# Kernel tuning notes

Hardware: AMD Instinct MI355X
Metric: run time of the kernel (lower is better)

The kernel has to match this reference:

```python
import jax, jax.numpy as jnp
import numpy as np

FEAT = 512
MATCH = 256
EPS = 1e-5

def layernorm(x, gamma, beta):
    mu = jnp.mean(x, axis=-1, keepdims=True)
    var = jnp.var(x, axis=-1, keepdims=True)
    return (x - mu) * jax.lax.rsqrt(var + EPS) * gamma + beta

def setup_inputs() -> dict:
    key = jax.random.key(0)
    ks = jax.random.split(key, 5)
    B, N = 8, 2048
    patch_corr_map = jax.random.normal(ks[0], (B, N, FEAT), dtype=jnp.float32)
    W_proj = jax.random.normal(ks[1], (FEAT, MATCH), dtype=jnp.float32) * (1.0 / np.sqrt(FEAT))
    b_proj = jnp.zeros((MATCH,), dtype=jnp.float32)
    g1 = jnp.ones((MATCH,), dtype=jnp.float32)
    be1 = jnp.zeros((MATCH,), dtype=jnp.float32)
    g2 = jnp.ones((FEAT,), dtype=jnp.float32)
    be2 = jnp.zeros((FEAT,), dtype=jnp.float32)
    W_out = jax.random.normal(ks[2], (FEAT, FEAT), dtype=jnp.float32) * (1.0 / np.sqrt(FEAT))
    b_out = jnp.zeros((FEAT,), dtype=jnp.float32)
    return {"patch_corr_map": patch_corr_map, "W_proj": W_proj, "b_proj": b_proj,
            "g1": g1, "be1": be1, "g2": g2, "be2": be2, "W_out": W_out, "b_out": b_out}

def reference(patch_corr_map, W_proj, b_proj, g1, be1, g2, be2, W_out, b_out):
    # Linear feat->match, then LayerNorm; q = k = normed projection
    proj = jnp.einsum('bnf,fm->bnm', patch_corr_map, W_proj) + b_proj
    qk = layernorm(proj, g1, be1)                      # [B,N,M]
    v = layernorm(patch_corr_map, g2, be2)             # [B,N,F]
    attn = jnp.einsum('bnm,bkm->bnk', qk, qk)          # [B,N,N], no scaling (matches torch)
    attn = jax.nn.softmax(attn, axis=-1)
    out = jnp.einsum('bnk,bkf->bnf', attn, v)          # [B,N,F]
    out = out + (jnp.einsum('bnf,fg->bng', out, W_out) + b_out)
    return out
```

## Files before the change

kernel.cpp:

```cpp
#include <hip/hip_runtime.h>
#include <hip/hip_bf16.h>
#include <cstdint>
#include <cstddef>

#define FEAT 512
#define MATCH 256
#define NB 8
#define NSEQ 2048
#define NROWS (NB*NSEQ)
#define LN_EPS 1e-5f

using f32x4  = __attribute__((ext_vector_type(4))) float;
using bf16x8 = __attribute__((ext_vector_type(8))) short;
using s16x4  = __attribute__((ext_vector_type(4))) short;
using i32x4  = __attribute__((ext_vector_type(4))) int;

__device__ __forceinline__ float bf2f(short h){
  return __builtin_bit_cast(float, (uint32_t)((uint32_t)(uint16_t)h << 16));
}
__device__ __forceinline__ short f2bf(float f){
  uint32_t u = __builtin_bit_cast(uint32_t, f);
  u += 0x7FFFu + ((u >> 16) & 1u);
  return (short)(u >> 16);
}
__device__ __forceinline__ int cvtpk(float a, float b){
  int d;
  asm("v_cvt_pk_bf16_f32 %0, %1, %2" : "=v"(d) : "v"(a), "v"(b));
  return d;
}
__device__ __forceinline__ void gl_lds16(const void* g, void* l){
  __builtin_amdgcn_global_load_lds(
    (const __attribute__((address_space(1))) uint32_t*)g,
    (__attribute__((address_space(3))) uint32_t*)l, 16, 0, 0);
}
#define MFMA16(a,b,c) __builtin_amdgcn_mfma_f32_16x16x32_bf16((a),(b),(c),0,0,0)

template<int ADDI>
__global__ void k_transpose_convert(const float* __restrict__ src, short* __restrict__ dst,
                                    int R, int C){
  __shared__ short tile[32][33];
  int tx = threadIdx.x, ty = threadIdx.y;
  int c0 = blockIdx.x * 32, r0 = blockIdx.y * 32;
#pragma unroll
  for (int r = 0; r < 4; r++){
    int gr = r0 + ty + 8*r, gc = c0 + tx;
    float v = src[(size_t)gr * C + gc];
    if (ADDI && gr == gc) v += 1.0f;
    tile[ty + 8*r][tx] = f2bf(v);
  }
  __syncthreads();
#pragma unroll
  for (int r = 0; r < 4; r++)
    dst[(size_t)(c0 + ty + 8*r) * R + r0 + tx] = tile[tx][ty + 8*r];
}

__launch_bounds__(512)
__global__ void k_prep2(const float* __restrict__ x, const float* __restrict__ g2,
                        const float* __restrict__ be2,
                        short* __restrict__ xbf, short* __restrict__ vT){
  __shared__ short vtile[32*FEAT];
  int t = threadIdx.x, l = t & 63, w = t >> 6;
  int b  = blockIdx.x >> 6;
  int n0 = (blockIdx.x & 63) * 32;
  float4 ga = ((const float4*)g2)[l*2],  gb = ((const float4*)g2)[l*2+1];
  float4 ea = ((const float4*)be2)[l*2], eb = ((const float4*)be2)[l*2+1];
#pragma unroll
  for (int r = 0; r < 4; r++){
    int rowL = w*4 + r;
    size_t row = (size_t)b * NSEQ + n0 + rowL;
    const float* xr = x + row * FEAT;
    float4 a = ((const float4*)xr)[l*2];
    float4 c = ((const float4*)xr)[l*2+1];
    float s  = a.x+a.y+a.z+a.w + c.x+c.y+c.z+c.w;
    float ss = a.x*a.x+a.y*a.y+a.z*a.z+a.w*a.w + c.x*c.x+c.y*c.y+c.z*c.z+c.w*c.w;
#pragma unroll
    for (int d = 1; d < 64; d <<= 1){ s += __shfl_xor(s, d); ss += __shfl_xor(ss, d); }
    float mu  = s * (1.f/FEAT);
    float var = ss * (1.f/FEAT) - mu*mu;
    float rs  = rsqrtf(var + LN_EPS);
    bf16x8 xv, vv;
    float xs[8] = {a.x,a.y,a.z,a.w,c.x,c.y,c.z,c.w};
    float gs[8] = {ga.x,ga.y,ga.z,ga.w,gb.x,gb.y,gb.z,gb.w};
    float es[8] = {ea.x,ea.y,ea.z,ea.w,eb.x,eb.y,eb.z,eb.w};
#pragma unroll
    for (int i = 0; i < 8; i++){
      xv[i] = f2bf(xs[i]);
      vv[i] = f2bf((xs[i]-mu)*rs*gs[i] + es[i]);
    }
    *(bf16x8*)(xbf + row*FEAT + l*8) = xv;
    *(bf16x8*)(vtile + rowL*FEAT + l*8) = vv;
  }
  __syncthreads();
  short col[32];
#pragma unroll
  for (int n = 0; n < 32; n++) col[n] = vtile[n*FEAT + t];
  short* dst = vT + (size_t)b * FEAT * NSEQ + (size_t)t * NSEQ + n0;
#pragma unroll
  for (int c = 0; c < 4; c++)
    *(bf16x8*)(dst + c*8) = *(bf16x8*)&col[c*8];
}

__launch_bounds__(256, 2)
__global__ void k_gemm_ln(const short* __restrict__ A, const short* __restrict__ BT,
                          const float* __restrict__ bias, const float* __restrict__ g1,
                          const float* __restrict__ be1, short* __restrict__ qkbf){
  __shared__ __align__(16) short lA[64*64];
  __shared__ __align__(16) short lB[256*64];
  __shared__ float red[2][64][2];
  int t = threadIdx.x, l = t & 63, w = t >> 6;
  int mq = w & 1, nq = w >> 1;
  int m0 = blockIdx.x * 64;
  f32x4 acc[2][8] = {};
  for (int k0 = 0; k0 < FEAT; k0 += 64){
#pragma unroll
    for (int i = 0; i < 2; i++){
      int c = w*2 + i;
      gl_lds16(A + (size_t)(m0 + 8*c + (l>>3))*FEAT + k0 + (l&7)*8, (char*)lA + c*1024);
    }
#pragma unroll
    for (int i = 0; i < 8; i++){
      int c = w*8 + i;
      gl_lds16(BT + (size_t)(8*c + (l>>3))*FEAT + k0 + (l&7)*8, (char*)lB + c*1024);
    }
    __syncthreads();
#pragma unroll
    for (int ks = 0; ks < 2; ks++){
      bf16x8 af[2], bfr[8];
#pragma unroll
      for (int i = 0; i < 2; i++)
        af[i] = *(const bf16x8*)&lA[(32*mq + 16*i + (l&15))*64 + ks*32 + (l>>4)*8];
#pragma unroll
      for (int j = 0; j < 8; j++)
        bfr[j] = *(const bf16x8*)&lB[(128*nq + 16*j + (l&15))*64 + ks*32 + (l>>4)*8];
#pragma unroll
      for (int i = 0; i < 2; i++)
#pragma unroll
        for (int j = 0; j < 8; j++)
          acc[i][j] = MFMA16(af[i], bfr[j], acc[i][j]);
    }
    __syncthreads();
  }
  float g1v[8], bev[8];
#pragma unroll
  for (int j = 0; j < 8; j++){
    int col = 128*nq + 16*j + (l&15);
    float bv = bias[col];
#pragma unroll
    for (int i = 0; i < 2; i++)
#pragma unroll
      for (int r = 0; r < 4; r++) acc[i][j][r] += bv;
    g1v[j] = g1[col]; bev[j] = be1[col];
  }
#pragma unroll
  for (int i = 0; i < 2; i++)
#pragma unroll
    for (int r = 0; r < 4; r++){
      float s = 0.f, ss = 0.f;
#pragma unroll
      for (int j = 0; j < 8; j++){ float c = acc[i][j][r]; s += c; ss += c*c; }
#pragma unroll
      for (int d = 1; d < 16; d <<= 1){ s += __shfl_xor(s, d); ss += __shfl_xor(ss, d); }
      if ((l & 15) == 0){
        int rowL = 32*mq + 16*i + 4*(l>>4) + r;
        red[nq][rowL][0] = s; red[nq][rowL][1] = ss;
      }
    }
  __syncthreads();
#pragma unroll
  for (int i = 0; i < 2; i++)
#pragma unroll
    for (int r = 0; r < 4; r++){
      int rowL = 32*mq + 16*i + 4*(l>>4) + r;
      float s  = red[0][rowL][0] + red[1][rowL][0];
      float ss = red[0][rowL][1] + red[1][rowL][1];
      float mu = s * (1.f/MATCH);
      float var = ss * (1.f/MATCH) - mu*mu;
      float rs = rsqrtf(var + LN_EPS);
      size_t rowg = (size_t)(m0 + rowL) * MATCH;
#pragma unroll
      for (int j = 0; j < 8; j++){
        int col = 128*nq + 16*j + (l&15);
        qkbf[rowg + col] = f2bf((acc[i][j][r] - mu)*rs*g1v[j] + bev[j]);
      }
    }
}

__global__ void k_gemm(const short* __restrict__ A, const short* __restrict__ BT,
                       const float* __restrict__ bias,
                       float* __restrict__ C, int Kdim, int Ncols){
  __shared__ __align__(16) short lA[128*64];
  __shared__ __align__(16) short lB[128*64];
  int t = threadIdx.x, l = t & 63, w = t >> 6;
  int mq = w & 1, nq = w >> 1;
  int m0 = blockIdx.x * 128, n0 = blockIdx.y * 128;
  f32x4 acc[4][4] = {};
  for (int k0 = 0; k0 < Kdim; k0 += 64){
#pragma unroll
    for (int it = 0; it < 4; it++){
      int c = w*4 + it;
      gl_lds16(A  + (size_t)(m0 + 8*c + (l>>3))*Kdim + k0 + (l&7)*8, (char*)lA + c*1024);
      gl_lds16(BT + (size_t)(n0 + 8*c + (l>>3))*Kdim + k0 + (l&7)*8, (char*)lB + c*1024);
    }
    __syncthreads();
#pragma unroll
    for (int ks = 0; ks < 2; ks++){
      bf16x8 af[4], bfr[4];
#pragma unroll
      for (int i = 0; i < 4; i++)
        af[i]  = *(const bf16x8*)&lA[(64*mq + 16*i + (l&15))*64 + ks*32 + (l>>4)*8];
#pragma unroll
      for (int j = 0; j < 4; j++)
        bfr[j] = *(const bf16x8*)&lB[(64*nq + 16*j + (l&15))*64 + ks*32 + (l>>4)*8];
#pragma unroll
      for (int i = 0; i < 4; i++)
#pragma unroll
        for (int j = 0; j < 4; j++)
          acc[i][j] = MFMA16(af[i], bfr[j], acc[i][j]);
    }
    __syncthreads();
  }
#pragma unroll
  for (int i = 0; i < 4; i++)
#pragma unroll
    for (int j = 0; j < 4; j++){
      int col = n0 + 64*nq + 16*j + (l&15);
      float bv = bias[col];
#pragma unroll
      for (int r = 0; r < 4; r++){
        int row = m0 + 64*mq + 16*i + ((l>>4)<<2) + r;
        C[(size_t)row*Ncols + col] = acc[i][j][r] + bv;
      }
    }
}

#define KVB5 64
#define NT5  (NSEQ/KVB5)

__device__ __forceinline__ void stage_K5(const char* qkb, int kv0, char* lKb, int w, int l){
#pragma unroll
  for (int i = 0; i < 4; i++){
    int c = w*4 + i;
    int row = 2*c + (l>>5);
    int col = ((l&31)*16) ^ ((row&15)<<4);
    gl_lds16(qkb + (size_t)(kv0+row)*512 + col, lKb + c*1024);
  }
}
__device__ __forceinline__ void stage_V5(const char* vTb, int kv0, char* lVb, int w, int l){
#pragma unroll
  for (int i = 0; i < 8; i++){
    int c = w*8 + i;
    int row = 8*c + (l>>3);
    int col = ((l&7)*16) ^ ((row&7)<<4);
    gl_lds16(vTb + (size_t)row*4096 + (size_t)kv0*2 + col, lVb + c*1024);
  }
}

__launch_bounds__(512)
__global__ void k_attn6(const short* __restrict__ qk, const short* __restrict__ vT,
                        short* __restrict__ obf){
  __shared__ __align__(16) char lds[140544];
  char*  Vb   = lds + 65536;
  char*  Pb   = lds + 131072;
  float* denL = (float*)(lds + 139264);
  float* invL = (float*)(lds + 140288);
  int tdx = threadIdx.x, l = tdx & 63, w = tdx >> 6;
  int g = l >> 4, q = l & 15;
  int b  = blockIdx.x & 7;
  int q0 = (blockIdx.x >> 3) * 64;
  int kvf = w & 3, qfp = w >> 2;
  int fq  = w;
  const char* qkb = (const char*)(qk + (size_t)b * NSEQ * MATCH);
  const char* vTb = (const char*)(vT + (size_t)b * FEAT * NSEQ);
  bf16x8 qfr[2][8];
#pragma unroll
  for (int j = 0; j < 2; j++){
    const char* qr = qkb + (size_t)(q0 + 16*(2*qfp+j) + q)*512 + g*16;
#pragma unroll
    for (int ks = 0; ks < 8; ks++) qfr[j][ks] = *(const bf16x8*)(qr + ks*64);
  }
  f32x4 accO[4][4] = {};
  float den0 = 0.f, den1 = 0.f;
  int pkq = (q & 7) << 4;

  stage_K5(qkb, 0, lds, w, l);
  asm volatile("s_waitcnt vmcnt(0)" ::: "memory");
  __builtin_amdgcn_s_barrier();
  for (int tt = 0; tt < NT5; tt++){
    const char* Kcur = lds + ((tt&1) ? 32768 : 0);
    char*       Knxt = lds + ((tt&1) ? 0 : 32768);
    stage_V5(vTb, tt*KVB5, Vb, w, l);
    __builtin_amdgcn_sched_barrier(0);
    stage_K5(qkb, (tt+1)*KVB5, Knxt, w, l);
    __builtin_amdgcn_sched_barrier(0);
    f32x4 s0 = {}, s1 = {};
    const char* krow = Kcur + (size_t)(16*kvf + q)*512;
#pragma unroll
    for (int ks = 0; ks < 8; ks++){
      bf16x8 kf = *(const bf16x8*)(krow + ((ks*64 + 16*g) ^ (q<<4)));
      s0 = MFMA16(kf, qfr[0][ks], s0);
      s1 = MFMA16(kf, qfr[1][ks], s1);
    }
    float p0[4], p1[4];
#pragma unroll
    for (int r = 0; r < 4; r++){ p0[r] = __expf(s0[r] - 256.0f);
                                 p1[r] = __expf(s1[r] - 256.0f); }
    den0 += (p0[0]+p0[1]) + (p0[2]+p0[3]);
    den1 += (p1[0]+p1[1]) + (p1[2]+p1[3]);
    {
      int2 w0; w0.x = cvtpk(p0[0], p0[1]); w0.y = cvtpk(p0[2], p0[3]);
      int2 w1; w1.x = cvtpk(p1[0], p1[1]); w1.y = cvtpk(p1[2], p1[3]);
      int qg0 = 32*qfp + q, qg1 = qg0 + 16;
      int kb  = 32*kvf + 8*g;
      *(int2*)(Pb + qg0*128 + (kb ^ pkq)) = w0;
      *(int2*)(Pb + qg1*128 + (kb ^ pkq)) = w1;
    }
    asm volatile("s_waitcnt vmcnt(4) lgkmcnt(0)" ::: "memory");
    __builtin_amdgcn_s_barrier();
    __builtin_amdgcn_sched_barrier(0);
    __builtin_amdgcn_s_setprio(1);
#pragma unroll
    for (int st = 0; st < 2; st++){
      bf16x8 pa[4];
      int kvb = (64*st + 16*g) ^ pkq;
#pragma unroll
      for (int qf = 0; qf < 4; qf++)
        pa[qf] = *(const bf16x8*)(Pb + (16*qf + q)*128 + kvb);
#pragma unroll
      for (int fn = 0; fn < 4; fn++){
        int frow = 64*fq + 16*fn + q;
        bf16x8 vf = *(const bf16x8*)(Vb + (size_t)frow*128 + ((64*st + 16*g) ^ pkq));
#pragma unroll
        for (int qf = 0; qf < 4; qf++)
          accO[qf][fn] = MFMA16(pa[qf], vf, accO[qf][fn]);
      }
    }
    __builtin_amdgcn_s_setprio(0);
    asm volatile("s_waitcnt vmcnt(0) lgkmcnt(0)" ::: "memory");
    __builtin_amdgcn_s_barrier();
    __builtin_amdgcn_sched_barrier(0);
  }
  den0 += __shfl_xor(den0, 16); den0 += __shfl_xor(den0, 32);
  den1 += __shfl_xor(den1, 16); den1 += __shfl_xor(den1, 32);
  if (g == 0){
    denL[(kvf*4 + 2*qfp    )*16 + q] = den0;
    denL[(kvf*4 + 2*qfp + 1)*16 + q] = den1;
  }
  __syncthreads();
  if (w == 0){
    float s = denL[(0*4 + (l>>4))*16 + (l&15)] + denL[(1*4 + (l>>4))*16 + (l&15)]
            + denL[(2*4 + (l>>4))*16 + (l&15)] + denL[(3*4 + (l>>4))*16 + (l&15)];
    invL[l] = 1.0f / s;
  }
  __syncthreads();
  float invr[4][4];
#pragma unroll
  for (int qf = 0; qf < 4; qf++)
#pragma unroll
    for (int rr = 0; rr < 4; rr++)
      invr[qf][rr] = invL[16*qf + 4*g + rr];
#pragma unroll
  for (int qf = 0; qf < 4; qf++)
#pragma unroll
    for (int fn = 0; fn < 4; fn++)
#pragma unroll
      for (int rr = 0; rr < 4; rr++){
        int row = q0 + 16*qf + 4*g + rr;
        int col = 64*fq + 16*fn + q;
        obf[((size_t)b * NSEQ + row) * FEAT + col] = f2bf(accO[qf][fn][rr] * invr[qf][rr]);
      }
}

extern "C" void kernel_launch(void* const* d_in, const int* in_sizes, int n_in,
                              void* d_out, int out_size, void* d_ws, size_t ws_size,
                              hipStream_t stream) {
  const float* x   = (const float*)d_in[0];
  const float* Wp  = (const float*)d_in[1];
  const float* bp  = (const float*)d_in[2];
  const float* g1  = (const float*)d_in[3];
  const float* be1 = (const float*)d_in[4];
  const float* g2  = (const float*)d_in[5];
  const float* be2 = (const float*)d_in[6];
  const float* Wo  = (const float*)d_in[7];
  const float* bo  = (const float*)d_in[8];
  float* out = (float*)d_out;

  char* ws = (char*)d_ws;
  short* xbf  = (short*)ws;
  short* vT   = (short*)(ws + 16777216);
  short* qkbf = (short*)(ws + 33554432);
  short* obf  = (short*)(ws + 41943040);
  short* WpT  = (short*)(ws + 58720256);
  short* WoT  = (short*)(ws + 58982400);

  dim3 tb(32, 8, 1);
  k_transpose_convert<0><<<dim3(MATCH/32, FEAT/32, 1), tb, 0, stream>>>(Wp, WpT, FEAT, MATCH);
  k_transpose_convert<1><<<dim3(FEAT/32,  FEAT/32, 1), tb, 0, stream>>>(Wo, WoT, FEAT, FEAT);
  k_prep2<<<NB * (NSEQ/32), 512, 0, stream>>>(x, g2, be2, xbf, vT);
  k_gemm_ln<<<NROWS/64, 256, 0, stream>>>(xbf, WpT, bp, g1, be1, qkbf);
  k_attn6<<<NB * (NSEQ/64), 512, 0, stream>>>(qkbf, vT, obf);
  k_gemm<<<dim3(NROWS/128, FEAT/128, 1), 256, 0, stream>>>(obf, WoT, bo, out, FEAT, FEAT);
}
```

Measured before the change: 130.0 us.

## Load K fragments into registers and double-buffer V and P tiles in LDS

The attention kernel stops staging K tiles through LDS. Each wave now loads its K fragments directly from global memory into registers and prefetches the next tile's fragments after the barrier. The freed LDS holds double-buffered V tiles and double-buffered P tiles, so the next V tile is loaded while the current one is consumed. This removes one wait inside the loop and the K LDS reads, in exchange for more VGPR pressure (launch bounds now ask for 2 blocks per CU) and more LDS.

```diff
diff --git a/kernel.cpp b/kernel.cpp
--- a/kernel.cpp
+++ b/kernel.cpp
@@ -236,16 +236,7 @@
 #define KVB5 64
 #define NT5  (NSEQ/KVB5)
 
-__device__ __forceinline__ void stage_K5(const char* qkb, int kv0, char* lKb, int w, int l){
-#pragma unroll
-  for (int i = 0; i < 4; i++){
-    int c = w*4 + i;
-    int row = 2*c + (l>>5);
-    int col = ((l&31)*16) ^ ((row&15)<<4);
-    gl_lds16(qkb + (size_t)(kv0+row)*512 + col, lKb + c*1024);
-  }
-}
-__device__ __forceinline__ void stage_V5(const char* vTb, int kv0, char* lVb, int w, int l){
+__device__ __forceinline__ void stage_Vb(const char* vTb, int kv0, char* lVb, int w, int l){
 #pragma unroll
   for (int i = 0; i < 8; i++){
     int c = w*8 + i;
@@ -255,14 +246,12 @@
   }
 }
 
-__launch_bounds__(512)
-__global__ void k_attn6(const short* __restrict__ qk, const short* __restrict__ vT,
-                        short* __restrict__ obf){
-  __shared__ __align__(16) char lds[140544];
-  char*  Vb   = lds + 65536;
-  char*  Pb   = lds + 131072;
-  float* denL = (float*)(lds + 139264);
-  float* invL = (float*)(lds + 140288);
+__launch_bounds__(512, 2)
+__global__ void k_attn11(const short* __restrict__ qk, const short* __restrict__ vT,
+                         short* __restrict__ obf){
+  __shared__ __align__(16) char lds[148736];
+  float* denL = (float*)(lds + 147456);
+  float* invL = (float*)(lds + 148480);
   int tdx = threadIdx.x, l = tdx & 63, w = tdx >> 6;
   int g = l >> 4, q = l & 15;
   int b  = blockIdx.x & 7;
@@ -281,24 +270,25 @@
   f32x4 accO[4][4] = {};
   float den0 = 0.f, den1 = 0.f;
   int pkq = (q & 7) << 4;
-
-  stage_K5(qkb, 0, lds, w, l);
+  const char* kb = qkb + (size_t)(16*kvf + q)*512 + g*16;
+  bf16x8 kf[8];
+
+  stage_Vb(vTb, 0, lds, w, l);
+#pragma unroll
+  for (int ks = 0; ks < 8; ks++) kf[ks] = *(const bf16x8*)(kb + ks*64);
   asm volatile("s_waitcnt vmcnt(0)" ::: "memory");
   __builtin_amdgcn_s_barrier();
   for (int tt = 0; tt < NT5; tt++){
-    const char* Kcur = lds + ((tt&1) ? 32768 : 0);
-    char*       Knxt = lds + ((tt&1) ? 0 : 32768);
-    stage_V5(vTb, tt*KVB5, Vb, w, l);
-    __builtin_amdgcn_sched_barrier(0);
-    stage_K5(qkb, (tt+1)*KVB5, Knxt, w, l);
+    const char* Vc = lds + ((tt&1)  ? 65536 : 0);
+    char*       Vn = lds + ((tt&1)  ? 0 : 65536);
+    char*       Pc = lds + 131072 + ((tt&1) ? 8192 : 0);
+    stage_Vb(vTb, (tt+1)*KVB5, Vn, w, l);
     __builtin_amdgcn_sched_barrier(0);
     f32x4 s0 = {}, s1 = {};
-    const char* krow = Kcur + (size_t)(16*kvf + q)*512;
 #pragma unroll
     for (int ks = 0; ks < 8; ks++){
-      bf16x8 kf = *(const bf16x8*)(krow + ((ks*64 + 16*g) ^ (q<<4)));
-      s0 = MFMA16(kf, qfr[0][ks], s0);
-      s1 = MFMA16(kf, qfr[1][ks], s1);
+      s0 = MFMA16(kf[ks], qfr[0][ks], s0);
+      s1 = MFMA16(kf[ks], qfr[1][ks], s1);
     }
     float p0[4], p1[4];
 #pragma unroll
@@ -310,13 +300,18 @@
       int2 w0; w0.x = cvtpk(p0[0], p0[1]); w0.y = cvtpk(p0[2], p0[3]);
       int2 w1; w1.x = cvtpk(p1[0], p1[1]); w1.y = cvtpk(p1[2], p1[3]);
       int qg0 = 32*qfp + q, qg1 = qg0 + 16;
-      int kb  = 32*kvf + 8*g;
-      *(int2*)(Pb + qg0*128 + (kb ^ pkq)) = w0;
-      *(int2*)(Pb + qg1*128 + (kb ^ pkq)) = w1;
-    }
-    asm volatile("s_waitcnt vmcnt(4) lgkmcnt(0)" ::: "memory");
+      int kb2 = 32*kvf + 8*g;
+      *(int2*)(Pc + qg0*128 + (kb2 ^ pkq)) = w0;
+      *(int2*)(Pc + qg1*128 + (kb2 ^ pkq)) = w1;
+    }
+    asm volatile("s_waitcnt lgkmcnt(0)" ::: "memory");
     __builtin_amdgcn_s_barrier();
     __builtin_amdgcn_sched_barrier(0);
+    {
+      const char* kbn = kb + (size_t)(tt+1)*KVB5*512;
+#pragma unroll
+      for (int ks = 0; ks < 8; ks++) kf[ks] = *(const bf16x8*)(kbn + ks*64);
+    }
     __builtin_amdgcn_s_setprio(1);
 #pragma unroll
     for (int st = 0; st < 2; st++){
@@ -324,11 +319,11 @@
       int kvb = (64*st + 16*g) ^ pkq;
 #pragma unroll
       for (int qf = 0; qf < 4; qf++)
-        pa[qf] = *(const bf16x8*)(Pb + (16*qf + q)*128 + kvb);
+        pa[qf] = *(const bf16x8*)(Pc + (16*qf + q)*128 + kvb);
 #pragma unroll
       for (int fn = 0; fn < 4; fn++){
         int frow = 64*fq + 16*fn + q;
-        bf16x8 vf = *(const bf16x8*)(Vb + (size_t)frow*128 + ((64*st + 16*g) ^ pkq));
+        bf16x8 vf = *(const bf16x8*)(Vc + (size_t)frow*128 + ((64*st + 16*g) ^ pkq));
 #pragma unroll
         for (int qf = 0; qf < 4; qf++)
           accO[qf][fn] = MFMA16(pa[qf], vf, accO[qf][fn]);
@@ -397,6 +392,6 @@
   k_transpose_convert<1><<<dim3(FEAT/32,  FEAT/32, 1), tb, 0, stream>>>(Wo, WoT, FEAT, FEAT);
   k_prep2<<<NB * (NSEQ/32), 512, 0, stream>>>(x, g2, be2, xbf, vT);
   k_gemm_ln<<<NROWS/64, 256, 0, stream>>>(xbf, WpT, bp, g1, be1, qkbf);
-  k_attn6<<<NB * (NSEQ/64), 512, 0, stream>>>(qkbf, vT, obf);
+  k_attn11<<<NB * (NSEQ/64), 512, 0, stream>>>(qkbf, vT, obf);
   k_gemm<<<dim3(NROWS/128, FEAT/128, 1), 256, 0, stream>>>(obf, WoT, bo, out, FEAT, FEAT);
 }
```

Result: slower. 169.1 us (+30.0%).
